# Kernel optimization log

Hardware: AMD Instinct MI355X
Metric: run time of the kernel (lower is better)

## Reference

```python
import jax, jax.numpy as jnp
import numpy as np

# Tier config (cumulative d_model [256,1024,2048], cumulative heads [4,12,24], d_k=64)
TIER_OWN = [256, 768, 1024]      # per-tier own hidden dims
HEAD_OUT = [256, 512, 768]       # n_heads_per_tier[i] * d_k
NHS = [4, 8, 12]
DKS = [64, 64, 64]
RANK = 8
IN_OFF = np.cumsum([0] + TIER_OWN)    # [0,256,1024,2048]
OUT_OFF = np.cumsum([0] + HEAD_OUT)   # [0,256,768,1536]


def _block_ut_weight(key, in_dims, out_dims):
    """Full (sum_in, sum_out) matrix with lower-triangular blocks zeroed."""
    io = np.cumsum([0] + list(in_dims))
    oo = np.cumsum([0] + list(out_dims))
    n = len(in_dims)
    mask = np.zeros((io[-1], oo[-1]), dtype=np.float32)
    for i in range(n):
        for j in range(i, n):
            mask[io[i]:io[i + 1], oo[j]:oo[j + 1]] = 1.0
    W = jax.random.normal(key, (io[-1], oo[-1]), dtype=jnp.float32) * 0.02
    return W * jnp.asarray(mask)


def setup_inputs() -> dict:
    key = jax.random.key(0)
    ks = jax.random.split(key, 16)
    B, T, D = 4, 1024, 2048
    x = jax.random.normal(ks[0], (B, T, D), dtype=jnp.float32)
    W_Q = _block_ut_weight(ks[1], TIER_OWN, HEAD_OUT)
    W_K = _block_ut_weight(ks[2], TIER_OWN, HEAD_OUT)
    W_V = _block_ut_weight(ks[3], TIER_OWN, HEAD_OUT)
    W_O = _block_ut_weight(ks[4], HEAD_OUT, TIER_OWN)
    # feedback for tiers 0 and 1 (tier 2 has no higher tiers)
    hi0 = TIER_OWN[1] + TIER_OWN[2]  # 1792
    hi1 = TIER_OWN[2]                # 1024
    FK0 = jax.random.normal(ks[5], (hi0, NHS[0] * RANK), dtype=jnp.float32) * 0.02
    PK0 = jax.random.normal(ks[6], (NHS[0], RANK, DKS[0]), dtype=jnp.float32) * 0.01
    FV0 = jax.random.normal(ks[7], (hi0, NHS[0] * RANK), dtype=jnp.float32) * 0.02
    PV0 = jax.random.normal(ks[8], (NHS[0], RANK, DKS[0]), dtype=jnp.float32) * 0.01
    FK1 = jax.random.normal(ks[9], (hi1, NHS[1] * RANK), dtype=jnp.float32) * 0.02
    PK1 = jax.random.normal(ks[10], (NHS[1], RANK, DKS[1]), dtype=jnp.float32) * 0.01
    FV1 = jax.random.normal(ks[11], (hi1, NHS[1] * RANK), dtype=jnp.float32) * 0.02
    PV1 = jax.random.normal(ks[12], (NHS[1], RANK, DKS[1]), dtype=jnp.float32) * 0.01
    return dict(x=x, W_Q=W_Q, W_K=W_K, W_V=W_V, W_O=W_O,
                FK0=FK0, PK0=PK0, FV0=FV0, PV0=PV0,
                FK1=FK1, PK1=PK1, FV1=FV1, PV1=PV1)


def _forward(x, W_Q, W_K, W_V, W_O, FK0, PK0, FV0, PV0, FK1, PK1, FV1, PV1):
    B, T, _ = x.shape
    Q_all = x @ W_Q
    K_all = x @ W_K
    V_all = x @ W_V
    causal = jnp.tril(jnp.ones((T, T), dtype=bool))
    fb = {0: (FK0, PK0, FV0, PV0), 1: (FK1, PK1, FV1, PV1)}
    head_outs = []
    for tier in range(3):
        nh, dk = NHS[tier], DKS[tier]
        dim = nh * dk
        o = int(OUT_OFF[tier])
        Q = Q_all[..., o:o + dim]
        K = K_all[..., o:o + dim]
        V = V_all[..., o:o + dim]
        if tier in fb:
            Fk, Pk, Fv, Pv = fb[tier]
            h_hi = x[..., int(IN_OFF[tier + 1]):]  # higher tiers' hidden
            c_k = (h_hi @ Fk).reshape(B, T, nh, RANK)
            K = K + jnp.einsum('bthr,hrd->bthd', c_k, Pk).reshape(B, T, dim)
            c_v = (h_hi @ Fv).reshape(B, T, nh, RANK)
            V = V + jnp.einsum('bthr,hrd->bthd', c_v, Pv).reshape(B, T, dim)
        Qh = Q.reshape(B, T, nh, dk).transpose(0, 2, 1, 3)
        Kh = K.reshape(B, T, nh, dk).transpose(0, 2, 1, 3)
        Vh = V.reshape(B, T, nh, dk).transpose(0, 2, 1, 3)
        scores = jnp.einsum('bhqd,bhkd->bhqk', Qh, Kh) / jnp.sqrt(jnp.float32(dk))
        scores = jnp.where(causal, scores, jnp.float32(-1e30))
        attn = jax.nn.softmax(scores, axis=-1)
        out = jnp.einsum('bhqk,bhkd->bhqd', attn, Vh)
        head_outs.append(out.transpose(0, 2, 1, 3).reshape(B, T, dim))
    return jnp.concatenate(head_outs, axis=-1) @ W_O


def reference(x, W_Q, W_K, W_V, W_O, FK0, PK0, FV0, PV0, FK1, PK1, FV1, PV1):
    return _forward(x, W_Q, W_K, W_V, W_O, FK0, PK0, FV0, PV0, FK1, PK1, FV1, PV1)
```

## Files before the change

### kernel.cpp

```cpp
#include <hip/hip_runtime.h>


typedef short bf16x8 __attribute__((ext_vector_type(8)));
typedef float floatx4 __attribute__((ext_vector_type(4)));

__device__ __forceinline__ unsigned short f2bf(float f) {
  unsigned u = __builtin_bit_cast(unsigned, f);
  u += 0x7fffu + ((u >> 16) & 1u);
  return (unsigned short)(u >> 16);
}

__device__ __forceinline__ void gload_lds16(const unsigned short* g, unsigned short* l) {
  __builtin_amdgcn_global_load_lds((const __attribute__((address_space(1))) unsigned int*)g,
                                   (__attribute__((address_space(3))) unsigned int*)l, 16, 0, 0);
}

__global__ __launch_bounds__(256) void k_prep(
    const float* __restrict__ x, unsigned short* __restrict__ X16,
    const float* __restrict__ WQ, const float* __restrict__ WK, const float* __restrict__ WV,
    const float* __restrict__ FK0, const float* __restrict__ PK0,
    const float* __restrict__ FV0, const float* __restrict__ PV0,
    const float* __restrict__ FK1, const float* __restrict__ PK1,
    const float* __restrict__ FV1, const float* __restrict__ PV1,
    unsigned short* __restrict__ WTQKV,
    const float* __restrict__ WO, unsigned short* __restrict__ WTO) {
  __shared__ float tile[32][33];
  __shared__ float Fs[32][9];
  __shared__ float Ps[8][32];
  const int bid = blockIdx.x;
  const int tid = threadIdx.x;
  if (bid < 8192) {
    int i = bid * 256 + tid;
    float4 v = ((const float4*)x)[i];
    union { unsigned short u[4]; uint2 v2; } o;
    o.u[0] = f2bf(v.x); o.u[1] = f2bf(v.y); o.u[2] = f2bf(v.z); o.u[3] = f2bf(v.w);
    ((uint2*)X16)[i] = o.v2;
    return;
  }
  const int tx = tid & 31, ty = tid >> 5;
  if (bid < 17408) {
    int t = bid - 8192;
    int k0 = (t & 63) * 32, n0 = (t >> 6) * 32;
    const float* src; int nboff;
    if (n0 < 1536)      { src = WQ; nboff = n0; }
    else if (n0 < 3072) { src = WK; nboff = n0 - 1536; }
    else                { src = WV; nboff = n0 - 3072; }
#pragma unroll
    for (int j = 0; j < 4; ++j) {
      int kk = ty + j * 8;
      tile[kk][tx] = src[(size_t)(k0 + kk) * 1536 + nboff + tx];
    }
    int corrsel = 0; const float* Fsrc = nullptr; const float* Psrc = nullptr;
    int h = 0, d0 = 0, fs = 0, koff = 0;
    if (n0 >= 1536) {
      bool isK = (n0 < 3072);
      int np0 = isK ? (n0 - 1536) : (n0 - 3072);
      if (np0 < 256) {
        if (k0 >= 256) { corrsel = 1; Fsrc = isK ? FK0 : FV0; Psrc = isK ? PK0 : PV0;
                         h = np0 >> 6; d0 = np0 & 63; fs = 32; koff = k0 - 256; }
      } else if (np0 < 768) {
        if (k0 >= 1024) { corrsel = 1; Fsrc = isK ? FK1 : FV1; Psrc = isK ? PK1 : PV1;
                          h = (np0 - 256) >> 6; d0 = (np0 - 256) & 63; fs = 64; koff = k0 - 1024; }
      }
    }
    if (corrsel) {
      Fs[tid >> 3][tid & 7] = Fsrc[(size_t)(koff + (tid >> 3)) * fs + h * 8 + (tid & 7)];
      Ps[tid >> 5][tid & 31] = Psrc[h * 512 + (tid >> 5) * 64 + d0 + (tid & 31)];
    }
    __syncthreads();
#pragma unroll
    for (int j = 0; j < 4; ++j) {
      int nn = ty + j * 8;
      float v = tile[tx][nn];
      if (corrsel) {
        float c = 0.f;
#pragma unroll
        for (int r = 0; r < 8; ++r) c += Fs[tx][r] * Ps[r][nn];
        v += c;
      }
      WTQKV[(size_t)(n0 + nn) * 2048 + k0 + tx] = f2bf(v);
    }
  } else {
    int t = bid - 17408;
    int k0 = (t % 48) * 32, n0 = (t / 48) * 32;
#pragma unroll
    for (int j = 0; j < 4; ++j)
      tile[ty + j * 8][tx] = WO[(size_t)(k0 + ty + j * 8) * 2048 + n0 + tx];
    __syncthreads();
#pragma unroll
    for (int j = 0; j < 4; ++j)
      WTO[(size_t)(n0 + ty + j * 8) * 1536 + k0 + tx] = f2bf(tile[tx][ty + j * 8]);
  }
}

template <bool OUT_BF16, int MODE>
__global__ __launch_bounds__(256) void k_gemm_bt(const unsigned short* __restrict__ A,
                                                 const unsigned short* __restrict__ Bt,
                                                 void* __restrict__ C, int M, int N, int K) {
  __shared__ unsigned short As[128 * 64];
  __shared__ unsigned short Bs[128 * 64];
  const int tid = threadIdx.x;
  const int wave = tid >> 6, lane = tid & 63;
  const int qd = lane >> 4, ln = lane & 15;
  const int idx = blockIdx.x;
  const int xcd = idx & 7, r = idx >> 3;
  int bx, by;
  if (MODE == 0) {
    if (r < 120) {
      int L = xcd * 120 + r;
      int scol = L / 192, q = L % 192;
      by = q / 6; bx = 6 + scol * 6 + q % 6;
    } else {
      int ms = xcd * 24 + (r - 120);
      if (ms < 128) { bx = 2 + (ms & 3); by = ms >> 2; }
      else          { int sh = ms - 128; bx = sh & 1; by = sh >> 1; }
    }
  } else {
    if (r < 32) {
      int L = xcd * 32 + r;
      int scol = L >> 7, q = L & 127;
      by = q >> 2; bx = 8 + scol * 4 + (q & 3);
    } else if (r < 56) {
      int m = xcd * 24 + (r - 32);
      bx = 2 + m % 6; by = m / 6;
    } else {
      int sh = xcd * 8 + (r - 56);
      bx = sh & 1; by = sh >> 1;
    }
  }
  const int bm = by * 128, bn = bx * 128;
  const int wr = wave >> 1, wc = wave & 1;
  int Keff;
  if (MODE == 0) Keff = (bn < 256) ? 256 : (bn < 768 ? 1024 : 2048);
  else           Keff = (bn < 256) ? 256 : (bn < 1024 ? 768 : 1536);
  floatx4 acc[4][4];
#pragma unroll
  for (int i = 0; i < 4; ++i)
#pragma unroll
    for (int j = 0; j < 4; ++j) acc[i][j] = (floatx4){0.f, 0.f, 0.f, 0.f};
  const int rl = lane >> 3;
  const int sg = (lane & 7) ^ rl;
  const unsigned short* gA = A + (size_t)(bm + wave * 32 + rl) * K + sg * 8;
  const unsigned short* gB = Bt + (size_t)(bn + wave * 32 + rl) * K + sg * 8;
  unsigned short* lA = As + wave * 2048;
  unsigned short* lB = Bs + wave * 2048;
  const int l7 = ln & 7;
  for (int k0 = 0; k0 < Keff; k0 += 64) {
    __syncthreads();
#pragma unroll
    for (int i = 0; i < 4; ++i) {
      gload_lds16(gA + (size_t)8 * i * K + k0, lA + i * 512);
      gload_lds16(gB + (size_t)8 * i * K + k0, lB + i * 512);
    }
    __syncthreads();
#pragma unroll
    for (int h = 0; h < 2; ++h) {
      bf16x8 af[4], bfr[4];
#pragma unroll
      for (int mi = 0; mi < 4; ++mi)
        af[mi] = *(const bf16x8*)(As + (wr * 64 + mi * 16 + ln) * 64 + ((h * 4 + qd) ^ l7) * 8);
#pragma unroll
      for (int ni = 0; ni < 4; ++ni)
        bfr[ni] = *(const bf16x8*)(Bs + (wc * 64 + ni * 16 + ln) * 64 + ((h * 4 + qd) ^ l7) * 8);
#pragma unroll
      for (int mi = 0; mi < 4; ++mi)
#pragma unroll
        for (int ni = 0; ni < 4; ++ni)
          acc[mi][ni] = __builtin_amdgcn_mfma_f32_16x16x32_bf16(af[mi], bfr[ni], acc[mi][ni], 0, 0, 0);
    }
  }
#pragma unroll
  for (int mi = 0; mi < 4; ++mi)
#pragma unroll
    for (int r2 = 0; r2 < 4; ++r2) {
      int row = bm + wr * 64 + mi * 16 + qd * 4 + r2;
#pragma unroll
      for (int ni = 0; ni < 4; ++ni) {
        int col = bn + wc * 64 + ni * 16 + ln;
        if (OUT_BF16)
          ((unsigned short*)C)[(size_t)row * N + col] = f2bf(acc[mi][ni][r2]);
        else
          ((float*)C)[(size_t)row * N + col] = acc[mi][ni][r2];
      }
    }
}

__global__ void k_transpose_v(const unsigned short* __restrict__ QKV,
                              unsigned short* __restrict__ VT) {
  __shared__ unsigned short t[64 * 65];
  const int tt = blockIdx.x * 64, dt = blockIdx.y * 64, b = blockIdx.z;
  const int tid = threadIdx.x;
  const int r = tid >> 3, c0 = (tid & 7) * 8;
#pragma unroll
  for (int i = 0; i < 2; ++i) {
    int tok = r + i * 32;
    union { uint4 v; unsigned short u[8]; } vv;
    vv.v = *(const uint4*)(QKV + (size_t)(b * 1024 + tt + tok) * 4608 + 3072 + dt + c0);
#pragma unroll
    for (int j = 0; j < 8; ++j) t[tok * 65 + c0 + j] = vv.u[j];
  }
  __syncthreads();
#pragma unroll
  for (int i = 0; i < 2; ++i) {
    int d = r + i * 32;
    union { uint4 v; unsigned short u[8]; } vv;
#pragma unroll
    for (int j = 0; j < 8; ++j) vv.u[j] = t[(c0 + j) * 65 + d];
    *(uint4*)(VT + ((size_t)b * 1536 + dt + d) * 1024 + tt + c0) = vv.v;
  }
}

#define LDP 136
__global__ __launch_bounds__(256) void k_attn(const unsigned short* __restrict__ QKV,
                                              const unsigned short* __restrict__ VT,
                                              unsigned short* __restrict__ Oout) {
  __shared__ unsigned short Ks[128 * 64];
  __shared__ unsigned short VTs[64 * 128];
  __shared__ unsigned short Pl[4][16 * LDP];
  const int tid = threadIdx.x;
  const int wave = tid >> 6, lane = tid & 63;
  const int qd = lane >> 4, ln = lane & 15;
  const int qb = (int)gridDim.x - 1 - (int)blockIdx.x;
  const int gh = blockIdx.y, b = blockIdx.z;
  const int T = 1024, LD = 4608;
  const size_t rowbase = (size_t)b * T * LD;
  const int qcol = 64 * gh, kcol = 1536 + 64 * gh;
  const unsigned short* VTg = VT + ((size_t)b * 1536 + 64 * gh) * 1024;
  const float SCALE = 0.18033688f;
  const int q0 = qb * 128 + wave * 16;

  bf16x8 aq[2][2];
#pragma unroll
  for (int j = 0; j < 2; ++j) {
    const unsigned short* qp = QKV + rowbase + (size_t)(q0 + j * 64 + ln) * LD + qcol;
    aq[j][0] = *(const bf16x8*)(qp + qd * 8);
    aq[j][1] = *(const bf16x8*)(qp + 32 + qd * 8);
  }
  floatx4 Oacc[2][4];
#pragma unroll
  for (int j = 0; j < 2; ++j)
#pragma unroll
    for (int i = 0; i < 4; ++i) Oacc[j][i] = (floatx4){0.f, 0.f, 0.f, 0.f};
  float l_lane[2] = {0.f, 0.f};

  const int rk = lane >> 3;
  const int gk = ((lane & 7) ^ rk) * 8;
  const unsigned short* gK = QKV + rowbase + (size_t)(wave * 32 + rk) * LD + kcol + gk;
  unsigned short* lK = Ks + wave * 32 * 64;
  const int rv = lane >> 4;
  const int cv = lane & 15;
  unsigned short* lV = VTs + wave * 16 * 128;
  const unsigned short* gVrow[4];
  int gvcol[4];
#pragma unroll
  for (int i = 0; i < 4; ++i) {
    int d = wave * 16 + 4 * i + rv;
    gVrow[i] = VTg + (size_t)d * 1024;
    gvcol[i] = (cv ^ (4 * i + rv)) * 8;
  }
  const int l7 = ln & 7;

  for (int jt = 0; jt <= qb; ++jt) {
    const int jk = jt * 128;
    const bool diag = (jt == qb);
    __syncthreads();
#pragma unroll
    for (int i = 0; i < 4; ++i) {
      gload_lds16(gK + (size_t)(jk + 8 * i) * LD, lK + i * 512);
      gload_lds16(gVrow[i] + jk + gvcol[i], lV + i * 512);
    }
    __syncthreads();

#pragma unroll
    for (int j = 0; j < 2; ++j) {
      const bool dj0 = diag && (j == 0);
      const int hmax = dj0 ? 4 : 8;
      floatx4 Sc[8];
#pragma unroll
      for (int h = 0; h < 8; ++h) {
        if (h >= hmax) continue;
        Sc[h] = (floatx4){0.f, 0.f, 0.f, 0.f};
        bf16x8 a0 = *(const bf16x8*)(Ks + (h * 16 + ln) * 64 + (qd ^ l7) * 8);
        bf16x8 a1 = *(const bf16x8*)(Ks + (h * 16 + ln) * 64 + ((4 + qd) ^ l7) * 8);
        Sc[h] = __builtin_amdgcn_mfma_f32_16x16x32_bf16(a0, aq[j][0], Sc[h], 0, 0, 0);
        Sc[h] = __builtin_amdgcn_mfma_f32_16x16x32_bf16(a1, aq[j][1], Sc[h], 0, 0, 0);
      }
      const int qrow = q0 + j * 64 + ln;
      unsigned short* pw = Pl[wave];
#pragma unroll
      for (int h = 0; h < 8; ++h) {
        if (h >= hmax) continue;
        union { unsigned short u[4]; uint2 v; } pk;
#pragma unroll
        for (int r = 0; r < 4; ++r) {
          float v = fminf(Sc[h][r] * SCALE, 80.f);
          float p = __builtin_amdgcn_exp2f(v);
          if (diag && (j == 0 || h >= 4)) {
            int key = jk + h * 16 + qd * 4 + r;
            if (key > qrow) p = 0.f;
          }
          l_lane[j] += p;
          pk.u[r] = f2bf(p);
        }
        *(uint2*)(pw + ln * LDP + h * 16 + qd * 4) = pk.v;
      }
      __asm__ volatile("s_waitcnt lgkmcnt(0)" ::: "memory");
      const int smax = dj0 ? 2 : 4;
      bf16x8 pa[4];
#pragma unroll
      for (int s = 0; s < 4; ++s) {
        if (s >= smax) continue;
        pa[s] = *(const bf16x8*)(pw + ln * LDP + s * 32 + qd * 8);
      }
#pragma unroll
      for (int nc = 0; nc < 4; ++nc) {
        const int d = nc * 16 + ln;
#pragma unroll
        for (int s = 0; s < 4; ++s) {
          if (s >= smax) continue;
          bf16x8 bv = *(const bf16x8*)(VTs + d * 128 + (((s * 4 + qd) ^ ln) & 15) * 8);
          Oacc[j][nc] = __builtin_amdgcn_mfma_f32_16x16x32_bf16(pa[s], bv, Oacc[j][nc], 0, 0, 0);
        }
      }
    }
  }
#pragma unroll
  for (int j = 0; j < 2; ++j) {
    float l = l_lane[j];
    l += __shfl_xor(l, 16, 64);
    l += __shfl_xor(l, 32, 64);
#pragma unroll
    for (int r = 0; r < 4; ++r) {
      float inv = 1.0f / __shfl(l, qd * 4 + r, 64);
      size_t row = (size_t)b * T + q0 + j * 64 + qd * 4 + r;
#pragma unroll
      for (int nc = 0; nc < 4; ++nc)
        Oout[row * 1536 + 64 * gh + nc * 16 + ln] = f2bf(Oacc[j][nc][r] * inv);
    }
  }
}

extern "C" void kernel_launch(void* const* d_in, const int* in_sizes, int n_in,
                              void* d_out, int out_size, void* d_ws, size_t ws_size,
                              hipStream_t stream) {
  (void)in_sizes; (void)n_in; (void)out_size; (void)ws_size;
  const float* x   = (const float*)d_in[0];
  const float* WQ  = (const float*)d_in[1];
  const float* WK  = (const float*)d_in[2];
  const float* WV  = (const float*)d_in[3];
  const float* WO  = (const float*)d_in[4];
  const float* FK0 = (const float*)d_in[5];
  const float* PK0 = (const float*)d_in[6];
  const float* FV0 = (const float*)d_in[7];
  const float* PV0 = (const float*)d_in[8];
  const float* FK1 = (const float*)d_in[9];
  const float* PK1 = (const float*)d_in[10];
  const float* FV1 = (const float*)d_in[11];
  const float* PV1 = (const float*)d_in[12];

  char* ws = (char*)d_ws;
  unsigned short* X16   = (unsigned short*)(ws + 0);
  unsigned short* VTb   = X16;
  unsigned short* WTQKV = (unsigned short*)(ws + 16777216);
  unsigned short* QKV   = (unsigned short*)(ws + 35651584);
  unsigned short* ATT   = (unsigned short*)(ws + 73400320);
  unsigned short* WTO   = (unsigned short*)(ws + 85983232);

  k_prep<<<20480, 256, 0, stream>>>(x, X16, WQ, WK, WV,
                                    FK0, PK0, FV0, PV0, FK1, PK1, FV1, PV1,
                                    WTQKV, WO, WTO);
  k_gemm_bt<true, 0><<<1152, 256, 0, stream>>>(X16, WTQKV, QKV, 4096, 4608, 2048);
  k_transpose_v<<<dim3(16, 24, 4), 256, 0, stream>>>(QKV, VTb);
  k_attn<<<dim3(8, 24, 4), 256, 0, stream>>>(QKV, VTb, ATT);
  k_gemm_bt<false, 1><<<512, 256, 0, stream>>>(ATT, WTO, d_out, 4096, 2048, 1536);
}
```

Before: 319.0 us.

## Fuse V transpose into QKV GEMM epilogue and reorder attention grid

Result: faster. 303.6 us (-4.8%).

```diff
diff --git a/kernel.cpp b/kernel.cpp
--- a/kernel.cpp
+++ b/kernel.cpp
@@ -96,7 +96,8 @@
 template <bool OUT_BF16, int MODE>
 __global__ __launch_bounds__(256) void k_gemm_bt(const unsigned short* __restrict__ A,
                                                  const unsigned short* __restrict__ Bt,
-                                                 void* __restrict__ C, int M, int N, int K) {
+                                                 void* __restrict__ C, int M, int N, int K,
+                                                 unsigned short* __restrict__ VTout) {
   __shared__ unsigned short As[128 * 64];
   __shared__ unsigned short Bs[128 * 64];
   const int tid = threadIdx.x;
@@ -169,44 +170,46 @@
           acc[mi][ni] = __builtin_amdgcn_mfma_f32_16x16x32_bf16(af[mi], bfr[ni], acc[mi][ni], 0, 0, 0);
     }
   }
-#pragma unroll
-  for (int mi = 0; mi < 4; ++mi)
-#pragma unroll
-    for (int r2 = 0; r2 < 4; ++r2) {
-      int row = bm + wr * 64 + mi * 16 + qd * 4 + r2;
+  if (MODE == 0 && bn >= 3072) {
+    __syncthreads();
+    unsigned short* tw = (wave < 2) ? (As + wave * 4096) : (Bs + (wave - 2) * 4096);
+#pragma unroll
+    for (int mi = 0; mi < 4; ++mi)
 #pragma unroll
       for (int ni = 0; ni < 4; ++ni) {
-        int col = bn + wc * 64 + ni * 16 + ln;
-        if (OUT_BF16)
-          ((unsigned short*)C)[(size_t)row * N + col] = f2bf(acc[mi][ni][r2]);
-        else
-          ((float*)C)[(size_t)row * N + col] = acc[mi][ni][r2];
-      }
-    }
-}
-
-__global__ void k_transpose_v(const unsigned short* __restrict__ QKV,
-                              unsigned short* __restrict__ VT) {
-  __shared__ unsigned short t[64 * 65];
-  const int tt = blockIdx.x * 64, dt = blockIdx.y * 64, b = blockIdx.z;
-  const int tid = threadIdx.x;
-  const int r = tid >> 3, c0 = (tid & 7) * 8;
-#pragma unroll
-  for (int i = 0; i < 2; ++i) {
-    int tok = r + i * 32;
-    union { uint4 v; unsigned short u[8]; } vv;
-    vv.v = *(const uint4*)(QKV + (size_t)(b * 1024 + tt + tok) * 4608 + 3072 + dt + c0);
-#pragma unroll
-    for (int j = 0; j < 8; ++j) t[tok * 65 + c0 + j] = vv.u[j];
-  }
-  __syncthreads();
-#pragma unroll
-  for (int i = 0; i < 2; ++i) {
-    int d = r + i * 32;
-    union { uint4 v; unsigned short u[8]; } vv;
-#pragma unroll
-    for (int j = 0; j < 8; ++j) vv.u[j] = t[(c0 + j) * 65 + d];
-    *(uint4*)(VT + ((size_t)b * 1536 + dt + d) * 1024 + tt + c0) = vv.v;
+        union { unsigned short u[4]; uint2 v; } p;
+#pragma unroll
+        for (int rr = 0; rr < 4; ++rr) p.u[rr] = f2bf(acc[mi][ni][rr]);
+        int d = ni * 16 + ln;
+        int c = mi * 2 + (qd >> 1);
+        *(uint2*)(tw + d * 64 + ((c ^ (ln & 7)) << 3) + ((qd & 1) << 2)) = p.v;
+      }
+    __asm__ volatile("s_waitcnt lgkmcnt(0)" ::: "memory");
+    const int a = lane >> 3, bl = lane & 7;
+    const int bb = bm >> 10, tt0 = bm & 1023;
+    const int dbase = (bn - 3072) + wc * 64;
+    const int tg = tt0 + wr * 64 + bl * 8;
+#pragma unroll
+    for (int i = 0; i < 8; ++i) {
+      int d = a + 8 * i;
+      uint4 v = *(const uint4*)(tw + d * 64 + ((bl ^ a) << 3));
+      *(uint4*)(VTout + ((size_t)(bb * 1536 + dbase + d)) * 1024 + tg) = v;
+    }
+  } else {
+#pragma unroll
+    for (int mi = 0; mi < 4; ++mi)
+#pragma unroll
+      for (int r2 = 0; r2 < 4; ++r2) {
+        int row = bm + wr * 64 + mi * 16 + qd * 4 + r2;
+#pragma unroll
+        for (int ni = 0; ni < 4; ++ni) {
+          int col = bn + wc * 64 + ni * 16 + ln;
+          if (OUT_BF16)
+            ((unsigned short*)C)[(size_t)row * N + col] = f2bf(acc[mi][ni][r2]);
+          else
+            ((float*)C)[(size_t)row * N + col] = acc[mi][ni][r2];
+        }
+      }
   }
 }
 
@@ -220,9 +223,9 @@
   const int tid = threadIdx.x;
   const int wave = tid >> 6, lane = tid & 63;
   const int qd = lane >> 4, ln = lane & 15;
-  const int qb = (int)gridDim.x - 1 - (int)blockIdx.x;
-  const int gh = blockIdx.y, b = blockIdx.z;
-  const int T = 1024, LD = 4608;
+  const int gh = blockIdx.x, b = blockIdx.y;
+  const int qb = 7 - (int)blockIdx.z;
+  const int T = 1024, LD = 3072;
   const size_t rowbase = (size_t)b * T * LD;
   const int qcol = 64 * gh, kcol = 1536 + 64 * gh;
   const unsigned short* VTg = VT + ((size_t)b * 1536 + 64 * gh) * 1024;
@@ -360,17 +363,16 @@
 
   char* ws = (char*)d_ws;
   unsigned short* X16   = (unsigned short*)(ws + 0);
-  unsigned short* VTb   = X16;
   unsigned short* WTQKV = (unsigned short*)(ws + 16777216);
-  unsigned short* QKV   = (unsigned short*)(ws + 35651584);
+  unsigned short* QK    = (unsigned short*)(ws + 35651584);
+  unsigned short* VT    = (unsigned short*)(ws + 60817408);
   unsigned short* ATT   = (unsigned short*)(ws + 73400320);
   unsigned short* WTO   = (unsigned short*)(ws + 85983232);
 
   k_prep<<<20480, 256, 0, stream>>>(x, X16, WQ, WK, WV,
                                     FK0, PK0, FV0, PV0, FK1, PK1, FV1, PV1,
                                     WTQKV, WO, WTO);
-  k_gemm_bt<true, 0><<<1152, 256, 0, stream>>>(X16, WTQKV, QKV, 4096, 4608, 2048);
-  k_transpose_v<<<dim3(16, 24, 4), 256, 0, stream>>>(QKV, VTb);
-  k_attn<<<dim3(8, 24, 4), 256, 0, stream>>>(QKV, VTb, ATT);
-  k_gemm_bt<false, 1><<<512, 256, 0, stream>>>(ATT, WTO, d_out, 4096, 2048, 1536);
-}
+  k_gemm_bt<true, 0><<<1152, 256, 0, stream>>>(X16, WTQKV, QK, 4096, 3072, 2048, VT);
+  k_attn<<<dim3(24, 4, 8), 256, 0, stream>>>(QK, VT, ATT);
+  k_gemm_bt<false, 1><<<512, 256, 0, stream>>>(ATT, WTO, d_out, 4096, 2048, 1536, nullptr);
+}
```
